# Optimization experiments

Measured on AMD Instinct MI355X. Metric: run time of the kernel, lower is better.

## Reference

```python
import jax, jax.numpy as jnp
import numpy as np

B, D, E = 16384, 2048, 16
MIN_K, MAX_K = 1, 4
H = D // 2  # hidden width of similarity/routing MLPs
TOP20 = int(0.2 * D)  # static: int(0.2 * x.shape[-1])


def _lin_init(k, fan_in, shape):
    bound = 1.0 / np.sqrt(fan_in)
    return jax.random.uniform(k, shape, jnp.float32, -bound, bound)


def setup_inputs() -> dict:
    key = jax.random.key(0)
    ks = jax.random.split(key, 16)
    return {
        'x': jax.random.normal(ks[0], (B, D), jnp.float32),
        'expert_patterns': jax.random.normal(ks[1], (E, D), jnp.float32),
        # similarity_network: Linear(D, D//2) -> ReLU -> Linear(D//2, E)
        'Ws1': _lin_init(ks[2], D, (D, H)), 'bs1': _lin_init(ks[3], D, (H,)),
        'Ws2': _lin_init(ks[4], H, (H, E)), 'bs2': _lin_init(ks[5], H, (E,)),
        # routing_network: Linear(D+E, D//2) -> ReLU -> (Dropout eval) -> Linear(D//2, E) -> Softmax
        'Wr1': _lin_init(ks[6], D + E, (D + E, H)), 'br1': _lin_init(ks[7], D + E, (H,)),
        'Wr2': _lin_init(ks[8], H, (H, E)), 'br2': _lin_init(ks[9], H, (E,)),
        # k_predictor: Linear(6,16) -> ReLU -> Linear(16,1) -> Sigmoid
        'Wk1': _lin_init(ks[10], 6, (6, 16)), 'bk1': _lin_init(ks[11], 6, (16,)),
        'Wk2': _lin_init(ks[12], 16, (16, 1)), 'bk2': _lin_init(ks[13], 16, (1,)),
    }


def _feature_analysis(x):
    mean = jnp.mean(x, axis=-1, keepdims=True)
    var_u = jnp.var(x, axis=-1, ddof=1)  # torch.var is unbiased
    std = jnp.sqrt(var_u[:, None] + 1e-8)
    skew = jnp.mean(((x - mean) / std) ** 3, axis=-1)
    ax = jnp.abs(x)
    sorted_ax = -jnp.sort(-ax, axis=-1)  # descending
    total = jnp.sum(sorted_ax, axis=-1)
    top = jnp.sum(sorted_ax[:, :TOP20], axis=-1)
    # stacked in DynamicTopKSelector order: sparsity,variance,magnitude,norm,skewness,concentration
    stats = jnp.stack([
        jnp.mean((x == 0).astype(jnp.float32), axis=-1),
        var_u,
        jnp.max(ax, axis=-1),
        jnp.linalg.norm(x, axis=-1),
        skew,
        top / (total + 1e-8),
    ], axis=-1)  # [B, 6]
    return stats


def _lower_median(v):
    # torch.median returns the lower of two middle elements for even n
    n = v.shape[0]
    return jnp.sort(v)[(n - 1) // 2]


def reference(x, expert_patterns, Ws1, bs1, Ws2, bs2, Wr1, br1, Wr2, br2, Wk1, bk1, Wk2, bk2):
    stats = _feature_analysis(x)  # [B, 6]
    # expert specialization
    sims = x @ expert_patterns.T                                  # [B, E]
    spec = jax.nn.relu(x @ Ws1 + bs1) @ Ws2 + bs2                 # [B, E]
    spec_scores = jax.nn.sigmoid(sims + spec)
    # routing network (dropout inactive in eval)
    ri = jnp.concatenate([x, spec_scores], axis=-1)               # [B, D+E]
    probs = jax.nn.softmax(jax.nn.relu(ri @ Wr1 + br1) @ Wr2 + br2, axis=-1)
    # dynamic top-k (host-side scalar in torch -> static-shape pad/mask here)
    k_ratio = jax.nn.sigmoid(jax.nn.relu(stats @ Wk1 + bk1) @ Wk2 + bk2)[:, 0]
    k_values = MIN_K + (MAX_K - MIN_K) * k_ratio
    k = jnp.clip(jnp.floor(_lower_median(k_values)).astype(jnp.int32), MIN_K, MAX_K)
    k = jax.lax.stop_gradient(k)
    topk_probs, topk_idx = jax.lax.top_k(probs, MAX_K)            # [B, MAX_K]
    mask = jnp.arange(MAX_K) < k                                  # first k slots active
    gates = jax.nn.softmax(jnp.where(mask, topk_probs, -1e30), axis=-1)
    return gates, topk_idx, probs, stats
```

## Files before the change

kernel.cpp:

```cpp
#include <hip/hip_runtime.h>
#include <hip/hip_bf16.h>

typedef unsigned short u16;
typedef __attribute__((ext_vector_type(8))) short bf16x8;
typedef __attribute__((ext_vector_type(8))) unsigned short u16x8;
typedef __attribute__((ext_vector_type(4))) float f32x4;

#define BB 16384
#define DD 2048
#define KEXT 2112
#define HH 1024
#define EE 16
#define TOPN 409

__device__ __forceinline__ u16 f2bf(float f) {
    union { float f; unsigned u; } c; c.f = f;
    unsigned r = c.u + 0x7fffu + ((c.u >> 16) & 1u);
    return (u16)(r >> 16);
}
__device__ __forceinline__ float bf2f(u16 h) {
    union { unsigned u; float f; } c; c.u = ((unsigned)h) << 16; return c.f;
}

__device__ __forceinline__ void ld16_lds(const void* g, void* l) {
    __builtin_amdgcn_global_load_lds(
        (const __attribute__((address_space(1))) unsigned int*)g,
        (__attribute__((address_space(3))) unsigned int*)l, 16, 0, 0);
}

__global__ __launch_bounds__(256)
void prep_t(const float* __restrict__ Ws1, const float* __restrict__ Wr1,
            u16* __restrict__ w1t, u16* __restrict__ wr1h, u16* __restrict__ wr1l)
{
    __shared__ float tile[64][65];
    const int kt = blockIdx.x;
    const int nt = blockIdx.y;
    const int mat = blockIdx.z;
    if (mat == 0 && kt >= 32) return;
    const int k0 = kt * 64, n0 = nt * 64;
    const float* src = mat ? Wr1 : Ws1;
    const int kmax = mat ? (DD + EE) : DD;
    const int t = threadIdx.x;
    #pragma unroll
    for (int i = 0; i < 16; ++i) {
        int e = i * 256 + t;
        int r = e >> 6, c = e & 63;
        float v = (k0 + r < kmax) ? src[(size_t)(k0 + r) * HH + n0 + c] : 0.0f;
        tile[r][c] = v;
    }
    __syncthreads();
    #pragma unroll
    for (int i = 0; i < 16; ++i) {
        int e = i * 256 + t;
        int rn = e >> 6, ck = e & 63;
        float v = tile[ck][rn];
        size_t oidx = (size_t)(n0 + rn) * KEXT + k0 + ck;
        if (mat == 0) {
            w1t[oidx] = f2bf(v);
        } else {
            u16 h = f2bf(v);
            wr1h[oidx] = h;
            wr1l[oidx] = f2bf(v - bf2f(h));
        }
    }
}

__global__ __launch_bounds__(256)
void prep_small(const float* __restrict__ Ws2, const float* __restrict__ Wr2,
                const float* __restrict__ pat,
                u16* __restrict__ w2t1, u16* __restrict__ wr2th, u16* __restrict__ wr2tl,
                u16* __restrict__ patTh, u16* __restrict__ patTl)
{
    int idx = blockIdx.x * 256 + threadIdx.x;
    if (idx < EE * HH) {
        int e = idx / HH, n = idx % HH;
        w2t1[idx] = f2bf(Ws2[(size_t)n * EE + e]);
        float v = Wr2[(size_t)n * EE + e];
        u16 h = f2bf(v);
        wr2th[idx] = h;
        wr2tl[idx] = f2bf(v - bf2f(h));
    }
    if (idx < EE * DD) {
        float v = pat[idx];
        u16 h = f2bf(v);
        patTh[idx] = h;
        patTl[idx] = f2bf(v - bf2f(h));
    }
}

__global__ __launch_bounds__(256)
void stats_kernel(const float* __restrict__ x,
                  const float* __restrict__ Wk1, const float* __restrict__ bk1,
                  const float* __restrict__ Wk2, const float* __restrict__ bk2,
                  float* __restrict__ stats_out, u16* __restrict__ xh, u16* __restrict__ xl,
                  unsigned* __restrict__ kflags)
{
    const int wid = threadIdx.x >> 6;
    const int lane = threadIdx.x & 63;
    const int row = blockIdx.x * 4 + wid;
    const float* xr = x + (size_t)row * DD;

    float v[32];
    #pragma unroll
    for (int s = 0; s < 8; ++s) {
        float4 a = *(const float4*)(xr + s * 256 + lane * 4);
        v[s*4+0]=a.x; v[s*4+1]=a.y; v[s*4+2]=a.z; v[s*4+3]=a.w;
    }

    u16* ph = xh + (size_t)row * KEXT;
    u16* pl = xl + (size_t)row * KEXT;
    #pragma unroll
    for (int s = 0; s < 8; ++s) {
        union { u16 a[4]; unsigned long long q; } H, L;
        #pragma unroll
        for (int c = 0; c < 4; ++c) {
            float f = v[s*4+c];
            u16 h = f2bf(f);
            H.a[c] = h; L.a[c] = f2bf(f - bf2f(h));
        }
        *(unsigned long long*)(ph + s*256 + lane*4) = H.q;
        *(unsigned long long*)(pl + s*256 + lane*4) = L.q;
    }
    ph[DD + lane] = 0;
    pl[DD + lane] = 0;

    float s1 = 0;
    #pragma unroll
    for (int j = 0; j < 32; ++j) s1 += v[j];
    #pragma unroll
    for (int off = 32; off >= 1; off >>= 1) s1 += __shfl_xor(s1, off);
    const float mean = s1 * (1.0f/2048.0f);

    float s2=0, s3=0, sa=0, sq=0, zc=0, mx=0;
    #pragma unroll
    for (int j = 0; j < 32; ++j) {
        float d = v[j] - mean;
        s2 += d*d; s3 += d*d*d;
        float av = fabsf(v[j]);
        sa += av; sq += v[j]*v[j];
        mx = fmaxf(mx, av);
        zc += (v[j] == 0.0f) ? 1.0f : 0.0f;
    }
    #pragma unroll
    for (int off = 32; off >= 1; off >>= 1) {
        s2 += __shfl_xor(s2, off);
        s3 += __shfl_xor(s3, off);
        sa += __shfl_xor(sa, off);
        sq += __shfl_xor(sq, off);
        zc += __shfl_xor(zc, off);
        mx = fmaxf(mx, __shfl_xor(mx, off));
    }

    #pragma unroll
    for (int j = 0; j < 32; ++j) v[j] = fabsf(v[j]);

    unsigned lo = 0, hi = 0x7F800000u;
    while (lo < hi) {
        unsigned mid = (lo + hi) >> 1;
        float midf = __uint_as_float(mid);
        unsigned cnt = 0;
        #pragma unroll
        for (int j = 0; j < 32; ++j)
            cnt += (unsigned)__popcll(__ballot(v[j] > midf));
        if (cnt < TOPN) hi = mid; else lo = mid + 1;
    }
    const float T = __uint_as_float(lo);

    float cg = 0, sg = 0;
    #pragma unroll
    for (int j = 0; j < 32; ++j) {
        if (v[j] > T) { cg += 1.0f; sg += v[j]; }
    }
    #pragma unroll
    for (int off = 32; off >= 1; off >>= 1) { cg += __shfl_xor(cg, off); sg += __shfl_xor(sg, off); }

    if (lane == 0) {
        float top = sg + ((float)TOPN - cg) * T;
        float var_u = s2 * (1.0f/2047.0f);
        float stdv = sqrtf(var_u + 1e-8f);
        float st0 = zc * (1.0f/2048.0f);
        float st1 = var_u;
        float st2 = mx;
        float st3 = sqrtf(sq);
        float st4 = (s3 * (1.0f/2048.0f)) / (stdv*stdv*stdv);
        float st5 = top / (sa + 1e-8f);
        float* so = stats_out + (size_t)row * 6;
        so[0]=st0; so[1]=st1; so[2]=st2; so[3]=st3; so[4]=st4; so[5]=st5;
        float stv[6] = {st0,st1,st2,st3,st4,st5};
        float o = bk2[0];
        #pragma unroll
        for (int i = 0; i < 16; ++i) {
            float h = bk1[i];
            #pragma unroll
            for (int f = 0; f < 6; ++f) h += stv[f] * Wk1[f*16 + i];
            o += fmaxf(h, 0.0f) * Wk2[i];
        }
        float kr = 1.0f / (1.0f + expf(-o));
        float kv = 1.0f + 3.0f * kr;
        kflags[row] = (kv < 2.0f ? 1u : 0u) | (kv < 3.0f ? 0x10000u : 0u);
    }
}

__global__ __launch_bounds__(1024)
void kmed_kernel(const unsigned* __restrict__ kflags, int* __restrict__ counters)
{
    const int t = threadIdx.x;
    unsigned s = 0;
    for (int i = t; i < BB; i += 1024) s += kflags[i];
    #pragma unroll
    for (int off = 32; off >= 1; off >>= 1) s += __shfl_xor(s, off);
    __shared__ unsigned red[16];
    if ((t & 63) == 0) red[t >> 6] = s;
    __syncthreads();
    if (t == 0) {
        unsigned tot = 0;
        #pragma unroll
        for (int w = 0; w < 16; ++w) tot += red[w];
        counters[0] = (int)(tot & 0xFFFFu);
        counters[1] = (int)(tot >> 16);
    }
}

template<bool SPLIT3, bool OSPLIT>
__global__ __launch_bounds__(256)
void gemm_tile(const u16* __restrict__ Ah, const u16* __restrict__ Al,
               const u16* __restrict__ Bh, const u16* __restrict__ Bl,
               const float* __restrict__ bias,
               u16* __restrict__ Oh, u16* __restrict__ Ol,
               int kiters, int stride)
{
    __shared__ u16 AsH[128*64];
    __shared__ u16 BsH[128*64];
    __shared__ u16 AsL[SPLIT3 ? 128*64 : 8];
    __shared__ u16 BsL[SPLIT3 ? 128*64 : 8];
    const int t = threadIdx.x;
    const int id = blockIdx.x;
    const int xcd = id & 7;
    const int jj = id >> 3;
    const int nblk = jj & 7;
    const int mgrp = jj >> 3;
    const int m0 = (xcd * 16 + mgrp) * 128;
    const int n0 = nblk * 128;
    const int wid = t >> 6, lane = t & 63, l16 = lane & 15, q = lane >> 4;
    const int wm = (wid & 1) * 64, wn = (wid >> 1) * 64;
    const int x7 = l16 & 7;

    f32x4 acc[4][4] = {};

    for (int it = 0; it < kiters; ++it) {
        const int k0 = it * 64;
        __syncthreads();
        #pragma unroll
        for (int s = 0; s < 4; ++s) {
            int seg = t + s * 256;
            int row = seg >> 3;
            int c = (seg & 7) ^ (row & 7);
            size_t goff = (size_t)k0 + c * 8;
            size_t aoff = (size_t)(m0 + row) * stride + goff;
            size_t boff = (size_t)(n0 + row) * stride + goff;
            ld16_lds(Ah + aoff, (void*)(AsH + seg * 8));
            ld16_lds(Bh + boff, (void*)(BsH + seg * 8));
            if constexpr (SPLIT3) {
                ld16_lds(Al + aoff, (void*)(AsL + seg * 8));
                ld16_lds(Bl + boff, (void*)(BsL + seg * 8));
            }
        }
        __syncthreads();
        #pragma unroll
        for (int h = 0; h < 2; ++h) {
            const int coff = ((4*h + q) ^ x7) * 8;
            bf16x8 afh[4], bfh[4], afl[4], bfl[4];
            #pragma unroll
            for (int i = 0; i < 4; ++i) {
                const int ra = (wm + 16*i + l16) * 64 + coff;
                const int rb = (wn + 16*i + l16) * 64 + coff;
                afh[i] = *(const bf16x8*)(AsH + ra);
                bfh[i] = *(const bf16x8*)(BsH + rb);
                if constexpr (SPLIT3) {
                    afl[i] = *(const bf16x8*)(AsL + ra);
                    bfl[i] = *(const bf16x8*)(BsL + rb);
                }
            }
            #pragma unroll
            for (int i = 0; i < 4; ++i)
                #pragma unroll
                for (int j = 0; j < 4; ++j) {
                    acc[i][j] = __builtin_amdgcn_mfma_f32_16x16x32_bf16(afh[i], bfh[j], acc[i][j], 0, 0, 0);
                    if constexpr (SPLIT3) {
                        acc[i][j] = __builtin_amdgcn_mfma_f32_16x16x32_bf16(afh[i], bfl[j], acc[i][j], 0, 0, 0);
                        acc[i][j] = __builtin_amdgcn_mfma_f32_16x16x32_bf16(afl[i], bfh[j], acc[i][j], 0, 0, 0);
                    }
                }
        }
    }
    #pragma unroll
    for (int j = 0; j < 4; ++j) {
        int col = n0 + wn + 16*j + l16;
        float bv = bias[col];
        #pragma unroll
        for (int i = 0; i < 4; ++i)
            #pragma unroll
            for (int r = 0; r < 4; ++r) {
                int row = m0 + wm + 16*i + q*4 + r;
                float vv = acc[i][j][r] + bv;
                vv = vv > 0.0f ? vv : 0.0f;
                u16 h = f2bf(vv);
                Oh[(size_t)row * HH + col] = h;
                if constexpr (OSPLIT) Ol[(size_t)row * HH + col] = f2bf(vv - bf2f(h));
            }
    }
}

__global__ __launch_bounds__(256)
void thinA(const u16* __restrict__ xh, const u16* __restrict__ xl,
           const u16* __restrict__ patTh, const u16* __restrict__ patTl,
           const u16* __restrict__ ha, const u16* __restrict__ w2t,
           const float* __restrict__ bs2,
           u16* __restrict__ xh_w, u16* __restrict__ xl_w)
{
    const int t = threadIdx.x;
    const int wid = t >> 6, lane = t & 63, l16 = lane & 15, q = lane >> 4;
    const int m0 = blockIdx.x * 16;
    f32x4 acc = {};
    for (int it = wid; it < 64; it += 4) {
        const int k0 = it * 32;
        bf16x8 a0 = *(const bf16x8*)(xh + (size_t)(m0 + l16) * KEXT + k0 + q*8);
        bf16x8 a1 = *(const bf16x8*)(xl + (size_t)(m0 + l16) * KEXT + k0 + q*8);
        bf16x8 b0 = *(const bf16x8*)(patTh + (size_t)l16 * DD + k0 + q*8);
        bf16x8 b1 = *(const bf16x8*)(patTl + (size_t)l16 * DD + k0 + q*8);
        acc = __builtin_amdgcn_mfma_f32_16x16x32_bf16(a0, b0, acc, 0, 0, 0);
        acc = __builtin_amdgcn_mfma_f32_16x16x32_bf16(a0, b1, acc, 0, 0, 0);
        acc = __builtin_amdgcn_mfma_f32_16x16x32_bf16(a1, b0, acc, 0, 0, 0);
    }
    for (int it = wid; it < 32; it += 4) {
        const int k0 = it * 32;
        bf16x8 a = *(const bf16x8*)(ha + (size_t)(m0 + l16) * HH + k0 + q*8);
        bf16x8 b = *(const bf16x8*)(w2t + (size_t)l16 * HH + k0 + q*8);
        acc = __builtin_amdgcn_mfma_f32_16x16x32_bf16(a, b, acc, 0, 0, 0);
    }
    __shared__ f32x4 red[4][64];
    red[wid][lane] = acc;
    __syncthreads();
    if (wid == 0) {
        f32x4 v = red[0][lane];
        #pragma unroll
        for (int w = 1; w < 4; ++w) {
            f32x4 o = red[w][lane];
            v[0]+=o[0]; v[1]+=o[1]; v[2]+=o[2]; v[3]+=o[3];
        }
        const float b2 = bs2[l16];
        #pragma unroll
        for (int r = 0; r < 4; ++r) {
            int row = m0 + q*4 + r;
            float ssv = 1.0f / (1.0f + expf(-(v[r] + b2)));
            u16 h = f2bf(ssv);
            u16 lo = f2bf(ssv - bf2f(h));
            xh_w[(size_t)row * KEXT + DD + l16] = h;
            xl_w[(size_t)row * KEXT + DD + l16] = lo;
        }
    }
}

__global__ __launch_bounds__(256)
void thinB(const u16* __restrict__ hh, const u16* __restrict__ hl,
           const u16* __restrict__ wr2th, const u16* __restrict__ wr2tl,
           const float* __restrict__ br2, const int* __restrict__ counters,
           float* __restrict__ out_gates, float* __restrict__ out_idx,
           float* __restrict__ out_probs)
{
    const int t = threadIdx.x;
    const int wid = t >> 6, lane = t & 63, l16 = lane & 15, q = lane >> 4;
    const int m0 = blockIdx.x * 16;
    f32x4 acc = {};
    for (int it = wid; it < 32; it += 4) {
        const int k0 = it * 32;
        bf16x8 a0 = *(const bf16x8*)(hh + (size_t)(m0 + l16) * HH + k0 + q*8);
        bf16x8 a1 = *(const bf16x8*)(hl + (size_t)(m0 + l16) * HH + k0 + q*8);
        bf16x8 b0 = *(const bf16x8*)(wr2th + (size_t)l16 * HH + k0 + q*8);
        bf16x8 b1 = *(const bf16x8*)(wr2tl + (size_t)l16 * HH + k0 + q*8);
        acc = __builtin_amdgcn_mfma_f32_16x16x32_bf16(a0, b0, acc, 0, 0, 0);
        acc = __builtin_amdgcn_mfma_f32_16x16x32_bf16(a0, b1, acc, 0, 0, 0);
        acc = __builtin_amdgcn_mfma_f32_16x16x32_bf16(a1, b0, acc, 0, 0, 0);
    }
    __shared__ f32x4 red[4][64];
    red[wid][lane] = acc;
    __syncthreads();
    if (wid != 0) return;
    f32x4 v = red[0][lane];
    #pragma unroll
    for (int w = 1; w < 4; ++w) {
        f32x4 o = red[w][lane];
        v[0]+=o[0]; v[1]+=o[1]; v[2]+=o[2]; v[3]+=o[3];
    }
    const float b2 = br2[l16];
    const int c2 = counters[0], c3 = counters[1];
    const int k = (c2 >= 8192) ? 1 : ((c3 >= 8192) ? 2 : 3);
    #pragma unroll
    for (int r = 0; r < 4; ++r) {
        const int row = m0 + q*4 + r;
        float lg = v[r] + b2;
        float mxv = lg;
        #pragma unroll
        for (int off = 1; off < 16; off <<= 1) mxv = fmaxf(mxv, __shfl_xor(mxv, off));
        float e = expf(lg - mxv);
        float den = e;
        #pragma unroll
        for (int off = 1; off < 16; off <<= 1) den += __shfl_xor(den, off);
        float p = e / den;
        out_probs[(size_t)row * EE + l16] = p;
        int kcur = (int)((__float_as_uint(p) & ~15u) | (15u - (unsigned)l16));
        float tv[4]; int ti[4];
        #pragma unroll
        for (int s = 0; s < 4; ++s) {
            int kk = kcur;
            #pragma unroll
            for (int off = 1; off < 16; off <<= 1) kk = max(kk, __shfl_xor(kk, off));
            int widx = 15 - (kk & 15);
            ti[s] = widx;
            tv[s] = __shfl(p, q * 16 + widx);
            if (l16 == widx) kcur = 0;
        }
        float den2 = 0.0f;
        float g[4];
        #pragma unroll
        for (int s = 0; s < 4; ++s) {
            g[s] = expf(tv[s] - tv[0]);
            if (s < k) den2 += g[s];
        }
        if (l16 < 4) {
            out_gates[(size_t)row * 4 + l16] = (l16 < k) ? g[l16] / den2 : 0.0f;
            out_idx[(size_t)row * 4 + l16] = (float)ti[l16];
        }
    }
}

extern "C" void kernel_launch(void* const* d_in, const int* in_sizes, int n_in,
                              void* d_out, int out_size, void* d_ws, size_t ws_size,
                              hipStream_t stream) {
    const float* x   = (const float*)d_in[0];
    const float* pat = (const float*)d_in[1];
    const float* Ws1 = (const float*)d_in[2];
    const float* bs1 = (const float*)d_in[3];
    const float* Ws2 = (const float*)d_in[4];
    const float* bs2 = (const float*)d_in[5];
    const float* Wr1 = (const float*)d_in[6];
    const float* br1 = (const float*)d_in[7];
    const float* Wr2 = (const float*)d_in[8];
    const float* br2 = (const float*)d_in[9];
    const float* Wk1 = (const float*)d_in[10];
    const float* bk1 = (const float*)d_in[11];
    const float* Wk2 = (const float*)d_in[12];
    const float* bk2 = (const float*)d_in[13];

    char* ws = (char*)d_ws;
    size_t off = 0;
    auto alloc = [&](size_t bytes) { char* p = ws + off; off += (bytes + 255) & ~(size_t)255; return p; };
    u16* xh     = (u16*)alloc((size_t)BB * KEXT * 2);
    u16* xl     = (u16*)alloc((size_t)BB * KEXT * 2);
    u16* w1t    = (u16*)alloc((size_t)HH * KEXT * 2);
    u16* wr1h   = (u16*)alloc((size_t)HH * KEXT * 2);
    u16* wr1l   = (u16*)alloc((size_t)HH * KEXT * 2);
    u16* w2t1   = (u16*)alloc((size_t)EE * HH * 2);
    u16* wr2th  = (u16*)alloc((size_t)EE * HH * 2);
    u16* wr2tl  = (u16*)alloc((size_t)EE * HH * 2);
    u16* patTh  = (u16*)alloc((size_t)EE * DD * 2);
    u16* patTl  = (u16*)alloc((size_t)EE * DD * 2);
    u16* ha     = (u16*)alloc((size_t)BB * HH * 2);
    u16* hb     = (u16*)alloc((size_t)BB * HH * 2);
    unsigned* kflags = (unsigned*)alloc((size_t)BB * 4);
    int* cnt      = (int*)alloc(64);

    float* out        = (float*)d_out;
    float* out_gates  = out;
    float* out_idx    = out + (size_t)BB * 4;
    float* out_probs  = out + (size_t)BB * 8;
    float* out_stats  = out + (size_t)BB * 24;

    prep_t<<<dim3(33, 16, 2), 256, 0, stream>>>(Ws1, Wr1, w1t, wr1h, wr1l);

    prep_small<<<(EE*DD + 255)/256, 256, 0, stream>>>(Ws2, Wr2, pat,
        w2t1, wr2th, wr2tl, patTh, patTl);

    stats_kernel<<<BB/4, 256, 0, stream>>>(x, Wk1, bk1, Wk2, bk2, out_stats, xh, xl, kflags);

    kmed_kernel<<<1, 1024, 0, stream>>>(kflags, cnt);

    gemm_tile<false, false><<<1024, 256, 0, stream>>>(
        xh, nullptr, w1t, nullptr, bs1, ha, nullptr, 32, KEXT);

    thinA<<<BB/16, 256, 0, stream>>>(xh, xl, patTh, patTl, ha, w2t1, bs2, xh, xl);

    gemm_tile<true, true><<<1024, 256, 0, stream>>>(
        xh, xl, wr1h, wr1l, br1, ha, hb, 33, KEXT);

    thinB<<<BB/16, 256, 0, stream>>>(ha, hb, wr2th, wr2tl, br2, cnt,
                                     out_gates, out_idx, out_probs);
}
```

Measured before the change: 628.2 us.

## Compute expert-pattern similarities in fp32 inside stats kernel instead of thinA

The x·pattern^T similarity product moves out of thinA's split-bf16 MFMA loop and into stats_kernel. It is computed in fp32 from the x values already in registers, with pattern tiles staged through LDS, and written to a small sims buffer that thinA adds before the sigmoid. This removes thinA's second read of xh/xl (about 134 MB) and the pattern split-precision prep. The cost is more ALU work and block syncs in stats_kernel, plus 16 cross-lane reductions per row.

```diff
diff --git a/kernel.cpp b/kernel.cpp
--- a/kernel.cpp
+++ b/kernel.cpp
@@ -67,34 +67,26 @@
 
 __global__ __launch_bounds__(256)
 void prep_small(const float* __restrict__ Ws2, const float* __restrict__ Wr2,
-                const float* __restrict__ pat,
-                u16* __restrict__ w2t1, u16* __restrict__ wr2th, u16* __restrict__ wr2tl,
-                u16* __restrict__ patTh, u16* __restrict__ patTl)
+                u16* __restrict__ w2t1, u16* __restrict__ wr2th, u16* __restrict__ wr2tl)
 {
     int idx = blockIdx.x * 256 + threadIdx.x;
-    if (idx < EE * HH) {
-        int e = idx / HH, n = idx % HH;
-        w2t1[idx] = f2bf(Ws2[(size_t)n * EE + e]);
-        float v = Wr2[(size_t)n * EE + e];
-        u16 h = f2bf(v);
-        wr2th[idx] = h;
-        wr2tl[idx] = f2bf(v - bf2f(h));
-    }
-    if (idx < EE * DD) {
-        float v = pat[idx];
-        u16 h = f2bf(v);
-        patTh[idx] = h;
-        patTl[idx] = f2bf(v - bf2f(h));
-    }
+    if (idx >= EE * HH) return;
+    int e = idx / HH, n = idx % HH;
+    w2t1[idx] = f2bf(Ws2[(size_t)n * EE + e]);
+    float v = Wr2[(size_t)n * EE + e];
+    u16 h = f2bf(v);
+    wr2th[idx] = h;
+    wr2tl[idx] = f2bf(v - bf2f(h));
 }
 
 __global__ __launch_bounds__(256)
-void stats_kernel(const float* __restrict__ x,
+void stats_kernel(const float* __restrict__ x, const float* __restrict__ pat,
                   const float* __restrict__ Wk1, const float* __restrict__ bk1,
                   const float* __restrict__ Wk2, const float* __restrict__ bk2,
                   float* __restrict__ stats_out, u16* __restrict__ xh, u16* __restrict__ xl,
-                  unsigned* __restrict__ kflags)
-{
+                  float* __restrict__ sims, unsigned* __restrict__ kflags)
+{
+    __shared__ float pat_lds[16 * 256];
     const int wid = threadIdx.x >> 6;
     const int lane = threadIdx.x & 63;
     const int row = blockIdx.x * 4 + wid;
@@ -123,6 +115,37 @@
     }
     ph[DD + lane] = 0;
     pl[DD + lane] = 0;
+
+    float sim[16];
+    #pragma unroll
+    for (int e = 0; e < 16; ++e) sim[e] = 0.0f;
+    for (int s = 0; s < 8; ++s) {
+        __syncthreads();
+        #pragma unroll
+        for (int k4 = 0; k4 < 4; ++k4) {
+            int fidx = k4 * 1024 + threadIdx.x * 4;
+            int e = fidx >> 8, col = fidx & 255;
+            *(float4*)(pat_lds + fidx) = *(const float4*)(pat + (size_t)e * DD + s * 256 + col);
+        }
+        __syncthreads();
+        #pragma unroll
+        for (int e = 0; e < 16; ++e) {
+            float4 pv = *(const float4*)(pat_lds + e * 256 + lane * 4);
+            sim[e] += v[s*4+0]*pv.x + v[s*4+1]*pv.y + v[s*4+2]*pv.z + v[s*4+3]*pv.w;
+        }
+    }
+    #pragma unroll
+    for (int e = 0; e < 16; ++e)
+        #pragma unroll
+        for (int off = 32; off >= 1; off >>= 1)
+            sim[e] += __shfl_xor(sim[e], off);
+    if (lane == 0) {
+        float4* sd = (float4*)(sims + (size_t)row * EE);
+        sd[0] = {sim[0],sim[1],sim[2],sim[3]};
+        sd[1] = {sim[4],sim[5],sim[6],sim[7]};
+        sd[2] = {sim[8],sim[9],sim[10],sim[11]};
+        sd[3] = {sim[12],sim[13],sim[14],sim[15]};
+    }
 
     float s1 = 0;
     #pragma unroll
@@ -312,26 +335,14 @@
 }
 
 __global__ __launch_bounds__(256)
-void thinA(const u16* __restrict__ xh, const u16* __restrict__ xl,
-           const u16* __restrict__ patTh, const u16* __restrict__ patTl,
-           const u16* __restrict__ ha, const u16* __restrict__ w2t,
-           const float* __restrict__ bs2,
+void thinA(const u16* __restrict__ ha, const u16* __restrict__ w2t,
+           const float* __restrict__ sims, const float* __restrict__ bs2,
            u16* __restrict__ xh_w, u16* __restrict__ xl_w)
 {
     const int t = threadIdx.x;
     const int wid = t >> 6, lane = t & 63, l16 = lane & 15, q = lane >> 4;
     const int m0 = blockIdx.x * 16;
     f32x4 acc = {};
-    for (int it = wid; it < 64; it += 4) {
-        const int k0 = it * 32;
-        bf16x8 a0 = *(const bf16x8*)(xh + (size_t)(m0 + l16) * KEXT + k0 + q*8);
-        bf16x8 a1 = *(const bf16x8*)(xl + (size_t)(m0 + l16) * KEXT + k0 + q*8);
-        bf16x8 b0 = *(const bf16x8*)(patTh + (size_t)l16 * DD + k0 + q*8);
-        bf16x8 b1 = *(const bf16x8*)(patTl + (size_t)l16 * DD + k0 + q*8);
-        acc = __builtin_amdgcn_mfma_f32_16x16x32_bf16(a0, b0, acc, 0, 0, 0);
-        acc = __builtin_amdgcn_mfma_f32_16x16x32_bf16(a0, b1, acc, 0, 0, 0);
-        acc = __builtin_amdgcn_mfma_f32_16x16x32_bf16(a1, b0, acc, 0, 0, 0);
-    }
     for (int it = wid; it < 32; it += 4) {
         const int k0 = it * 32;
         bf16x8 a = *(const bf16x8*)(ha + (size_t)(m0 + l16) * HH + k0 + q*8);
@@ -352,7 +363,8 @@
         #pragma unroll
         for (int r = 0; r < 4; ++r) {
             int row = m0 + q*4 + r;
-            float ssv = 1.0f / (1.0f + expf(-(v[r] + b2)));
+            float sarg = v[r] + sims[(size_t)row * EE + l16] + b2;
+            float ssv = 1.0f / (1.0f + expf(-sarg));
             u16 h = f2bf(ssv);
             u16 lo = f2bf(ssv - bf2f(h));
             xh_w[(size_t)row * KEXT + DD + l16] = h;
@@ -463,10 +475,9 @@
     u16* w2t1   = (u16*)alloc((size_t)EE * HH * 2);
     u16* wr2th  = (u16*)alloc((size_t)EE * HH * 2);
     u16* wr2tl  = (u16*)alloc((size_t)EE * HH * 2);
-    u16* patTh  = (u16*)alloc((size_t)EE * DD * 2);
-    u16* patTl  = (u16*)alloc((size_t)EE * DD * 2);
     u16* ha     = (u16*)alloc((size_t)BB * HH * 2);
     u16* hb     = (u16*)alloc((size_t)BB * HH * 2);
+    float* sims = (float*)alloc((size_t)BB * EE * 4);
     unsigned* kflags = (unsigned*)alloc((size_t)BB * 4);
     int* cnt      = (int*)alloc(64);
 
@@ -478,17 +489,17 @@
 
     prep_t<<<dim3(33, 16, 2), 256, 0, stream>>>(Ws1, Wr1, w1t, wr1h, wr1l);
 
-    prep_small<<<(EE*DD + 255)/256, 256, 0, stream>>>(Ws2, Wr2, pat,
-        w2t1, wr2th, wr2tl, patTh, patTl);
-
-    stats_kernel<<<BB/4, 256, 0, stream>>>(x, Wk1, bk1, Wk2, bk2, out_stats, xh, xl, kflags);
+    prep_small<<<(EE*HH + 255)/256, 256, 0, stream>>>(Ws2, Wr2, w2t1, wr2th, wr2tl);
+
+    stats_kernel<<<BB/4, 256, 0, stream>>>(x, pat, Wk1, bk1, Wk2, bk2,
+                                           out_stats, xh, xl, sims, kflags);
 
     kmed_kernel<<<1, 1024, 0, stream>>>(kflags, cnt);
 
     gemm_tile<false, false><<<1024, 256, 0, stream>>>(
         xh, nullptr, w1t, nullptr, bs1, ha, nullptr, 32, KEXT);
 
-    thinA<<<BB/16, 256, 0, stream>>>(xh, xl, patTh, patTl, ha, w2t1, bs2, xh, xl);
+    thinA<<<BB/16, 256, 0, stream>>>(ha, w2t1, sims, bs2, xh, xl);
 
     gemm_tile<true, true><<<1024, 256, 0, stream>>>(
         xh, xl, wr1h, wr1l, br1, ha, hb, 33, KEXT);
```

Result: slower. 680.9 us (+8.4%).
